# Kernel optimization log

Measured on AMD Instinct MI355X. Metric: run time of the kernel, lower is better.

Reference implementation:

```python
import jax, jax.numpy as jnp
import numpy as np

MAX_S, MIN_S, MAX_R = 3.0, 0.5, 3.0
A = (MAX_S - MIN_S) / 2.0   # 1.25
B = (MAX_S + MIN_S) / 2.0   # 1.75
C = (MAX_R - 1.0) / 2.0     # 1.0
D = (MAX_R + 1.0) / 2.0     # 2.0

# 3x3 kernel base points, row-major: dim0 = dy, dim1 = dx, shape [2, 9]
BASE = jnp.array([[-1, -1], [-1, 0], [-1, 1], [0, -1], [0, 0], [0, 1],
                  [1, -1], [1, 0], [1, 1]], dtype=jnp.float32).T


def conv2d(x, w, b=None):
    y = jax.lax.conv_general_dilated(x, w, window_strides=(1, 1),
                                     padding=((1, 1), (1, 1)),
                                     dimension_numbers=('NCHW', 'OIHW', 'NCHW'))
    if b is not None:
        y = y + b[None, :, None, None]
    return y


def setup_inputs() -> dict:
    key = jax.random.key(0)
    ks = jax.random.split(key, 8)
    return {
        'x': jax.random.normal(ks[0], (8, 64, 128, 128), jnp.float32),
        'w_main': jax.random.normal(ks[1], (64, 64, 3, 3), jnp.float32) * 0.05,
        'w_rot': jax.random.normal(ks[2], (2, 64, 3, 3), jnp.float32) * 0.05,
        'b_rot': jax.random.normal(ks[3], (2,), jnp.float32) * 0.05,
        'w_str': jax.random.normal(ks[4], (1, 64, 3, 3), jnp.float32) * 0.05,
        'b_str': jax.random.normal(ks[5], (1,), jnp.float32) * 0.05,
        'w_whl': jax.random.normal(ks[6], (1, 64, 3, 3), jnp.float32) * 0.05,
        'b_whl': jax.random.normal(ks[7], (1,), jnp.float32) * 0.05,
    }


def reference(x, w_main, w_rot, b_rot, w_str, b_str, w_whl, b_whl):
    b, c, H, W = x.shape
    K = 9
    # --- offset generation ---
    rot = conv2d(x, w_rot, b_rot)                     # [b,2,H,W]
    sin, cos = rot[:, 0], rot[:, 1]
    norm = jnp.sqrt(sin ** 2 + cos ** 2 + 1e-6)
    sin, cos = sin / norm, cos / norm
    r = jnp.tanh(conv2d(x, w_str, b_str))[:, 0] * A + B   # [b,H,W]
    wr = jnp.tanh(conv2d(x, w_whl, b_whl))[:, 0] * C + D  # [b,H,W]
    ky, kx = BASE[0], BASE[1]                             # [9]
    kyb = ky[None, :, None, None]
    kxb = kx[None, :, None, None]
    o0 = kyb * (wr * r)[:, None]                          # [b,9,H,W]
    o1 = kxb * wr[:, None]
    sinb, cosb = sin[:, None], cos[:, None]
    dy = cosb * o0 + sinb * o1 - kyb                      # rotation then subtract base
    dx = -sinb * o0 + cosb * o1 - kxb
    # --- deformable sampling positions (stride=1, pad=1, dil=1) ---
    py = jnp.arange(H, dtype=x.dtype)[None, None, :, None] + kyb + dy  # [b,9,H,W]
    px = jnp.arange(W, dtype=x.dtype)[None, None, None, :] + kxb + dx
    y0f = jnp.floor(py); x0f = jnp.floor(px)
    ly = py - y0f; lx = px - x0f
    y0 = y0f.astype(jnp.int32); x0 = x0f.astype(jnp.int32)
    x_flat = x.reshape(b, c, H * W)

    def gather(yi, xi, wgt):
        valid = (yi >= 0) & (yi < H) & (xi >= 0) & (xi < W)
        idx = jnp.clip(yi, 0, H - 1) * W + jnp.clip(xi, 0, W - 1)
        g = jnp.take_along_axis(x_flat, idx.reshape(b, 1, -1), axis=2)
        g = g.reshape(b, c, K, H, W)
        return g * (wgt * valid)[:, None]

    val = (gather(y0, x0, (1 - ly) * (1 - lx))
           + gather(y0, x0 + 1, (1 - ly) * lx)
           + gather(y0 + 1, x0, ly * (1 - lx))
           + gather(y0 + 1, x0 + 1, ly * lx))          # [b,c,9,H,W]
    # final 3x3 conv over sampled points == contraction over (c, k)
    out = jnp.einsum('bckhw,ock->bohw', val, w_main.reshape(w_main.shape[0], c, K))
    return out
```

## Files before the change

### kernel.cpp

```cpp
#include <hip/hip_runtime.h>
#include <hip/hip_bf16.h>
#include <hip/hip_fp16.h>
#include <math.h>

#define HH 128
#define WW 128
#define HWSZ (HH*WW)
#define CH 64
#define OC 64
#define NB 8
#define RG 28
#define RPX (RG*RG)

#define XT_BYTES   (16777216u)
#define OFFS_BYTES (2097152u)

typedef _Float16 f16x8 __attribute__((ext_vector_type(8)));
typedef __attribute__((ext_vector_type(4))) float f32x4_t;

__global__ __launch_bounds__(256) void pre_kernel(
    const float* __restrict__ x, const float* __restrict__ w_main,
    const float* __restrict__ w_rot, const float* __restrict__ w_str,
    const float* __restrict__ w_whl,
    __half* __restrict__ xT, __half* __restrict__ wmT2,
    float4* __restrict__ part)
{
    __shared__ float shmem[64 * 65];
    const int t = threadIdx.x;
    const int i = blockIdx.x;

    if (i >= 6144) {
        const int base = (i - 6144) * 4096 + t * 16;
        #pragma unroll
        for (int j = 0; j < 16; ++j) {
            const int e = base + j;
            const int k = e >> 12;
            const int r = e & 4095;
            const int o = r >> 6;
            const int c = r & 63;
            wmT2[e] = __float2half(w_main[(size_t)o * (CH * 9) + c * 9 + k]);
        }
        return;
    }

    if (i >= 4096) {
        float (*tile)[65] = (float(*)[65])shmem;
        const int it = i - 4096;
        const int b = it & 7;
        const int j = it >> 3;
        const int h  = j >> 1;
        const int w0 = (j & 1) * 64;
        const float* xb = x + (size_t)b * CH * HWSZ + h * WW + w0;
        {
            const int w = t & 63, c0 = (t >> 6) * 16;
            #pragma unroll
            for (int jj = 0; jj < 16; ++jj)
                tile[c0 + jj][w] = xb[(size_t)(c0 + jj) * HWSZ + w];
        }
        __syncthreads();
        {
            const int c = t & 63, wq = t >> 6;
            __half* o = xT + ((size_t)b * HWSZ + h * WW + w0) * 64;
            #pragma unroll
            for (int jj = 0; jj < 16; ++jj) {
                const int w = wq * 16 + jj;
                o[(size_t)w * 64 + c] = __float2half(tile[c][w]);
            }
        }
        return;
    }

    float (*xs)[4][WW] = (float(*)[4][WW])shmem;
    const int b  = i & 7;
    const int rp = (i >> 3) & 63;
    const int cg = i >> 9;
    const int h0 = rp * 2;
    const int c0 = cg * 8;
    const float* xb = x + (size_t)b * CH * HWSZ;
    #pragma unroll
    for (int jj = 0; jj < 4; ++jj) {
        const int u   = t + jj * 256;
        const int ch  = u >> 7;
        const int rem = u & 127;
        const int row = rem >> 5;
        const int w4  = (rem & 31) * 4;
        const int grow = h0 - 1 + row;
        float4 v = make_float4(0.f, 0.f, 0.f, 0.f);
        if (grow >= 0 && grow < HH)
            v = *(const float4*)&xb[((size_t)(c0 + ch) * HH + grow) * WW + w4];
        *(float4*)&xs[ch][row][w4] = v;
    }
    __syncthreads();
    const int r = t >> 7, w = t & 127;
    const int wl = max(w - 1, 0), wr2 = min(w + 1, WW - 1);
    const float ml = (w > 0) ? 1.f : 0.f, mr = (w < WW - 1) ? 1.f : 0.f;
    float a0 = 0.f, a1 = 0.f, a2 = 0.f, a3 = 0.f;
    #pragma unroll
    for (int ch = 0; ch < 8; ++ch) {
        const int cc = c0 + ch;
        #pragma unroll
        for (int dy = 0; dy < 3; ++dy) {
            const float* row_ = &xs[ch][r + dy][0];
            const float nl = row_[wl] * ml;
            const float nc = row_[w];
            const float nr = row_[wr2] * mr;
            const int d0 = cc * 9 + dy * 3;
            a0 = fmaf(nl, w_rot[d0 + 0], a0); a0 = fmaf(nc, w_rot[d0 + 1], a0); a0 = fmaf(nr, w_rot[d0 + 2], a0);
            a1 = fmaf(nl, w_rot[576 + d0 + 0], a1); a1 = fmaf(nc, w_rot[576 + d0 + 1], a1); a1 = fmaf(nr, w_rot[576 + d0 + 2], a1);
            a2 = fmaf(nl, w_str[d0 + 0], a2); a2 = fmaf(nc, w_str[d0 + 1], a2); a2 = fmaf(nr, w_str[d0 + 2], a2);
            a3 = fmaf(nl, w_whl[d0 + 0], a3); a3 = fmaf(nc, w_whl[d0 + 1], a3); a3 = fmaf(nr, w_whl[d0 + 2], a3);
        }
    }
    part[((size_t)cg * NB + b) * HWSZ + (h0 + r) * WW + w] = make_float4(a0, a1, a2, a3);
}

__global__ __launch_bounds__(256) void reduce_kernel(
    const float4* __restrict__ part,
    const float* __restrict__ b_rot, const float* __restrict__ b_str,
    const float* __restrict__ b_whl, float4* __restrict__ offs)
{
    const int i = blockIdx.x * 256 + threadIdx.x;
    float4 s = make_float4(0.f, 0.f, 0.f, 0.f);
    #pragma unroll
    for (int cg = 0; cg < 8; ++cg) {
        const float4 p = part[(size_t)cg * NB * HWSZ + i];
        s.x += p.x; s.y += p.y; s.z += p.z; s.w += p.w;
    }
    float sv = s.x + b_rot[0], cv = s.y + b_rot[1];
    const float inv = 1.0f / sqrtf(sv * sv + cv * cv + 1e-6f);
    const float rr = tanhf(s.z + b_str[0]) * 1.25f + 1.75f;
    const float wq = tanhf(s.w + b_whl[0]) * 1.0f + 2.0f;
    offs[i] = make_float4(sv * inv, cv * inv, wq * rr, wq);
}

__global__ __launch_bounds__(256, 3) void deform_kernel(
    const __half* __restrict__ xT, const __half* __restrict__ wmT2,
    const float4* __restrict__ offs, float* __restrict__ out)
{
    __shared__ union {
        uint4 xs[RPX * 4];
        float ots[64][67];
    } sh;
    const int t  = threadIdx.x;
    const int wv = t >> 6;
    const int l  = t & 63;
    const int lm = l & 15;
    const int lg = l >> 4;
    const int i  = blockIdx.x;
    const int b  = i & 7;
    const int tile = i >> 3;
    const int w0 = (tile & 15) * 8;
    const int h0 = (tile >> 4) * 8;
    const int pi = wv * 16 + lm;
    const int h = h0 + (pi >> 3);
    const int w = w0 + (pi & 7);
    const float4 o4 = offs[(size_t)b * HWSZ + h * WW + w];
    const float sv = o4.x, cv = o4.y, av = o4.z, wvl = o4.w;
    const float hh  = (float)h;
    const float wwf = (float)w;
    const __half* xb = xT + (size_t)b * HWSZ * 64;

    int ti[9], td[9];
    __half2 w2[9][4];
    #pragma unroll
    for (int k = 0; k < 9; ++k) {
        const float kyf = (float)(k / 3) - 1.f;
        const float kxf = (float)(k % 3) - 1.f;
        const float o0v = kyf * av;
        const float o1v = kxf * wvl;
        const float pyf = hh  + cv * o0v + sv * o1v;
        const float pxf = wwf - sv * o0v + cv * o1v;
        const float y0f = floorf(pyf), x0f = floorf(pxf);
        const float ly = pyf - y0f, lx = pxf - x0f;
        const int y0 = (int)y0f, x0i = (int)x0f;
        const int y1 = y0 + 1, x1 = x0i + 1;
        const bool vy0 = (y0 >= 0) && (y0 < HH);
        const bool vy1 = (y1 >= 0) && (y1 < HH);
        const bool vx0 = (x0i >= 0) && (x0i < WW);
        const bool vx1 = (x1 >= 0) && (x1 < WW);
        w2[k][0] = __float2half2_rn((1.f - ly) * (1.f - lx) * ((vy0 && vx0) ? 1.f : 0.f));
        w2[k][1] = __float2half2_rn((1.f - ly) * lx         * ((vy0 && vx1) ? 1.f : 0.f));
        w2[k][2] = __float2half2_rn(ly * (1.f - lx)         * ((vy1 && vx0) ? 1.f : 0.f));
        w2[k][3] = __float2half2_rn(ly * lx                 * ((vy1 && vx1) ? 1.f : 0.f));
        const int iy0 = min(max(y0, 0), HH - 1), iy1 = min(max(y1, 0), HH - 1);
        const int ix0 = min(max(x0i, 0), WW - 1), ix1 = min(max(x1, 0), WW - 1);
        ti[k] = (iy0 - (h0 - 10)) * RG + (ix0 - (w0 - 10));
        td[k] = (ix1 - ix0) | ((iy1 - iy0) << 1);
    }

    f32x4_t acc0 = {0.f, 0.f, 0.f, 0.f};
    f32x4_t acc1 = acc0, acc2 = acc0, acc3 = acc0;

    auto compute = [&](int g) {
        const int cb0 = g * 32 + lg * 8;
        const __half* wb = wmT2 + lm * 64 + cb0;
        f16x8 bc0 = *(const f16x8*)(wb);
        f16x8 bc1 = *(const f16x8*)(wb + 1024);
        f16x8 bc2 = *(const f16x8*)(wb + 2048);
        f16x8 bc3 = *(const f16x8*)(wb + 3072);
        #pragma unroll
        for (int k = 0; k < 9; ++k) {
            f16x8 bn0, bn1, bn2, bn3;
            if (k < 8) {
                const __half* wp = wb + (size_t)(k + 1) * 4096;
                bn0 = *(const f16x8*)(wp);
                bn1 = *(const f16x8*)(wp + 1024);
                bn2 = *(const f16x8*)(wp + 2048);
                bn3 = *(const f16x8*)(wp + 3072);
            }
            const int i00 = ti[k];
            const int dxx = td[k] & 1;
            const int dyy = (td[k] >> 1) * RG;
            const int i01 = i00 + dxx;
            const int i10 = i00 + dyy;
            const int i11 = i10 + dxx;
            union Q { uint4 q; __half2 h2[4]; };
            Q q00, q01, q10, q11;
            q00.q = sh.xs[i00 * 4 + (lg ^ ((i00 >> 1) & 3))];
            q01.q = sh.xs[i01 * 4 + (lg ^ ((i01 >> 1) & 3))];
            q10.q = sh.xs[i10 * 4 + (lg ^ ((i10 >> 1) & 3))];
            q11.q = sh.xs[i11 * 4 + (lg ^ ((i11 >> 1) & 3))];
            union { __half2 h2[4]; f16x8 v; } af;
            #pragma unroll
            for (int j = 0; j < 4; ++j) {
                const __half2 e0 = __hfma2(q00.h2[j], w2[k][0], __hmul2(q01.h2[j], w2[k][1]));
                const __half2 e1 = __hfma2(q10.h2[j], w2[k][2], __hmul2(q11.h2[j], w2[k][3]));
                af.h2[j] = __hadd2(e0, e1);
            }
            acc0 = __builtin_amdgcn_mfma_f32_16x16x32_f16(af.v, bc0, acc0, 0, 0, 0);
            acc1 = __builtin_amdgcn_mfma_f32_16x16x32_f16(af.v, bc1, acc1, 0, 0, 0);
            acc2 = __builtin_amdgcn_mfma_f32_16x16x32_f16(af.v, bc2, acc2, 0, 0, 0);
            acc3 = __builtin_amdgcn_mfma_f32_16x16x32_f16(af.v, bc3, acc3, 0, 0, 0);
            if (k < 8) { bc0 = bn0; bc1 = bn1; bc2 = bn2; bc3 = bn3; }
        }
    };

    for (int g = 0; g < 2; ++g) {
        __syncthreads();
        for (int u = t; u < RPX * 4; u += 256) {
            const int pxu = u >> 2, q = u & 3;
            const int lr = pxu / RG;
            const int lc = pxu - lr * RG;
            const int gy = min(max(h0 - 10 + lr, 0), HH - 1);
            const int gx = min(max(w0 - 10 + lc, 0), WW - 1);
            sh.xs[pxu * 4 + (q ^ ((pxu >> 1) & 3))] =
                *(const uint4*)(xb + (size_t)(gy * WW + gx) * 64 + g * 32 + q * 8);
        }
        __syncthreads();
        compute(g);
    }

    __syncthreads();
    const int pxw = wv * 16 + lg * 4;
    #pragma unroll
    for (int rg2 = 0; rg2 < 4; ++rg2) {
        sh.ots[pxw + rg2][ 0 + lm] = acc0[rg2];
        sh.ots[pxw + rg2][16 + lm] = acc1[rg2];
        sh.ots[pxw + rg2][32 + lm] = acc2[rg2];
        sh.ots[pxw + rg2][48 + lm] = acc3[rg2];
    }
    __syncthreads();
    const int oo = t >> 2;
    const int q  = (t & 3) * 16;
    #pragma unroll
    for (int j2 = 0; j2 < 4; ++j2) {
        const int px = q + j2 * 4;
        float4 v = make_float4(sh.ots[px + 0][oo], sh.ots[px + 1][oo],
                               sh.ots[px + 2][oo], sh.ots[px + 3][oo]);
        *(float4*)&out[((size_t)b * OC + oo) * HWSZ +
                       (h0 + (px >> 3)) * WW + w0 + (px & 7)] = v;
    }
}

extern "C" void kernel_launch(void* const* d_in, const int* in_sizes, int n_in,
                              void* d_out, int out_size, void* d_ws, size_t ws_size,
                              hipStream_t stream)
{
    const float* x      = (const float*)d_in[0];
    const float* w_main = (const float*)d_in[1];
    const float* w_rot  = (const float*)d_in[2];
    const float* b_rot  = (const float*)d_in[3];
    const float* w_str  = (const float*)d_in[4];
    const float* b_str  = (const float*)d_in[5];
    const float* w_whl  = (const float*)d_in[6];
    const float* b_whl  = (const float*)d_in[7];
    float* out = (float*)d_out;

    char* ws = (char*)d_ws;
    __half*  xT   = (__half*)ws;
    float4*  offs = (float4*)(ws + XT_BYTES);
    __half*  wmT2 = (__half*)(ws + XT_BYTES + OFFS_BYTES);
    float4*  part = (float4*)d_out;

    pre_kernel<<<dim3(6153), 256, 0, stream>>>(x, w_main, w_rot, w_str, w_whl,
                                               xT, wmT2, part);
    reduce_kernel<<<dim3(NB * HWSZ / 256), 256, 0, stream>>>(
        part, b_rot, b_str, b_whl, offs);
    deform_kernel<<<dim3(2048), 256, 0, stream>>>(xT, wmT2, offs, out);
}
```

Before: 205.3 us.

## Split channel staging into four 16-channel passes with 16x16x16 MFMA

The deform kernel now stages the input halo in four 16-channel chunks (8-byte entries) instead of two 32-channel chunks. It switches from the 16x16x32 MFMA to the 16x16x16 MFMA, drops the software prefetch of weight fragments, and raises the launch-bounds occupancy hint from 3 to 5 blocks per SM. The aim is to cut register pressure and raise occupancy. In exchange it doubles the number of halo reloads and barriers and issues twice as many smaller MFMAs and weight loads. It also changes the shared-memory swizzle.

```diff
diff --git a/kernel.cpp b/kernel.cpp
--- a/kernel.cpp
+++ b/kernel.cpp
@@ -15,7 +15,7 @@
 #define XT_BYTES   (16777216u)
 #define OFFS_BYTES (2097152u)
 
-typedef _Float16 f16x8 __attribute__((ext_vector_type(8)));
+typedef _Float16 f16x4 __attribute__((ext_vector_type(4)));
 typedef __attribute__((ext_vector_type(4))) float f32x4_t;
 
 __global__ __launch_bounds__(256) void pre_kernel(
@@ -133,12 +133,12 @@
     offs[i] = make_float4(sv * inv, cv * inv, wq * rr, wq);
 }
 
-__global__ __launch_bounds__(256, 3) void deform_kernel(
+__global__ __launch_bounds__(256, 5) void deform_kernel(
     const __half* __restrict__ xT, const __half* __restrict__ wmT2,
     const float4* __restrict__ offs, float* __restrict__ out)
 {
     __shared__ union {
-        uint4 xs[RPX * 4];
+        uint2 xs8[RPX * 4];
         float ots[64][67];
     } sh;
     const int t  = threadIdx.x;
@@ -191,63 +191,51 @@
     f32x4_t acc0 = {0.f, 0.f, 0.f, 0.f};
     f32x4_t acc1 = acc0, acc2 = acc0, acc3 = acc0;
 
-    auto compute = [&](int g) {
-        const int cb0 = g * 32 + lg * 8;
-        const __half* wb = wmT2 + lm * 64 + cb0;
-        f16x8 bc0 = *(const f16x8*)(wb);
-        f16x8 bc1 = *(const f16x8*)(wb + 1024);
-        f16x8 bc2 = *(const f16x8*)(wb + 2048);
-        f16x8 bc3 = *(const f16x8*)(wb + 3072);
+    for (int g = 0; g < 4; ++g) {
+        __syncthreads();
+        for (int u = t; u < RPX * 4; u += 256) {
+            const int pxu = u >> 2, s = u & 3;
+            const int lr = pxu / RG;
+            const int lc = pxu - lr * RG;
+            const int gy = min(max(h0 - 10 + lr, 0), HH - 1);
+            const int gx = min(max(w0 - 10 + lc, 0), WW - 1);
+            const int q4 = s ^ (pxu & 3);
+            sh.xs8[u] = *(const uint2*)(xb + (size_t)(gy * WW + gx) * 64 + g * 16 + q4 * 4);
+        }
+        __syncthreads();
+        const int cb0 = g * 16 + lg * 4;
         #pragma unroll
         for (int k = 0; k < 9; ++k) {
-            f16x8 bn0, bn1, bn2, bn3;
-            if (k < 8) {
-                const __half* wp = wb + (size_t)(k + 1) * 4096;
-                bn0 = *(const f16x8*)(wp);
-                bn1 = *(const f16x8*)(wp + 1024);
-                bn2 = *(const f16x8*)(wp + 2048);
-                bn3 = *(const f16x8*)(wp + 3072);
-            }
             const int i00 = ti[k];
             const int dxx = td[k] & 1;
             const int dyy = (td[k] >> 1) * RG;
             const int i01 = i00 + dxx;
             const int i10 = i00 + dyy;
             const int i11 = i10 + dxx;
-            union Q { uint4 q; __half2 h2[4]; };
+            union Q { uint2 q; __half2 h2[2]; };
             Q q00, q01, q10, q11;
-            q00.q = sh.xs[i00 * 4 + (lg ^ ((i00 >> 1) & 3))];
-            q01.q = sh.xs[i01 * 4 + (lg ^ ((i01 >> 1) & 3))];
-            q10.q = sh.xs[i10 * 4 + (lg ^ ((i10 >> 1) & 3))];
-            q11.q = sh.xs[i11 * 4 + (lg ^ ((i11 >> 1) & 3))];
-            union { __half2 h2[4]; f16x8 v; } af;
+            q00.q = sh.xs8[i00 * 4 + (lg ^ (i00 & 3))];
+            q01.q = sh.xs8[i01 * 4 + (lg ^ (i01 & 3))];
+            q10.q = sh.xs8[i10 * 4 + (lg ^ (i10 & 3))];
+            q11.q = sh.xs8[i11 * 4 + (lg ^ (i11 & 3))];
+            union { __half2 h2[2]; f16x4 v; } af;
             #pragma unroll
-            for (int j = 0; j < 4; ++j) {
-                const __half2 e0 = __hfma2(q00.h2[j], w2[k][0], __hmul2(q01.h2[j], w2[k][1]));
-                const __half2 e1 = __hfma2(q10.h2[j], w2[k][2], __hmul2(q11.h2[j], w2[k][3]));
-                af.h2[j] = __hadd2(e0, e1);
+            for (int j = 0; j < 2; ++j) {
+                af.h2[j] = __hfma2(q00.h2[j], w2[k][0],
+                           __hfma2(q01.h2[j], w2[k][1],
+                           __hfma2(q10.h2[j], w2[k][2],
+                           __hmul2(q11.h2[j], w2[k][3]))));
             }
-            acc0 = __builtin_amdgcn_mfma_f32_16x16x32_f16(af.v, bc0, acc0, 0, 0, 0);
-            acc1 = __builtin_amdgcn_mfma_f32_16x16x32_f16(af.v, bc1, acc1, 0, 0, 0);
-            acc2 = __builtin_amdgcn_mfma_f32_16x16x32_f16(af.v, bc2, acc2, 0, 0, 0);
-            acc3 = __builtin_amdgcn_mfma_f32_16x16x32_f16(af.v, bc3, acc3, 0, 0, 0);
-            if (k < 8) { bc0 = bn0; bc1 = bn1; bc2 = bn2; bc3 = bn3; }
-        }
-    };
-
-    for (int g = 0; g < 2; ++g) {
-        __syncthreads();
-        for (int u = t; u < RPX * 4; u += 256) {
-            const int pxu = u >> 2, q = u & 3;
-            const int lr = pxu / RG;
-            const int lc = pxu - lr * RG;
-            const int gy = min(max(h0 - 10 + lr, 0), HH - 1);
-            const int gx = min(max(w0 - 10 + lc, 0), WW - 1);
-            sh.xs[pxu * 4 + (q ^ ((pxu >> 1) & 3))] =
-                *(const uint4*)(xb + (size_t)(gy * WW + gx) * 64 + g * 32 + q * 8);
-        }
-        __syncthreads();
-        compute(g);
+            const __half* wp = wmT2 + ((size_t)k * 64 + lm) * 64 + cb0;
+            const f16x4 bf0 = *(const f16x4*)(wp);
+            const f16x4 bf1 = *(const f16x4*)(wp + 1024);
+            const f16x4 bf2v = *(const f16x4*)(wp + 2048);
+            const f16x4 bf3 = *(const f16x4*)(wp + 3072);
+            acc0 = __builtin_amdgcn_mfma_f32_16x16x16f16(af.v, bf0,  acc0, 0, 0, 0);
+            acc1 = __builtin_amdgcn_mfma_f32_16x16x16f16(af.v, bf1,  acc1, 0, 0, 0);
+            acc2 = __builtin_amdgcn_mfma_f32_16x16x16f16(af.v, bf2v, acc2, 0, 0, 0);
+            acc3 = __builtin_amdgcn_mfma_f32_16x16x16f16(af.v, bf3,  acc3, 0, 0, 0);
+        }
     }
 
     __syncthreads();
```

After: 297.8 us. 1.45x slower.
